# Kernel optimization log

Measured on AMD Instinct MI355X. Metric: run time of the kernel, lower is better.

The kernel has to match this reference:

```python
import jax, jax.numpy as jnp
import numpy as np

TEMPERATURE = 0.1
NEG_INF = -1e30  # finite sentinel to keep logsumexp grad-safe


def setup_inputs() -> dict:
    key = jax.random.key(0)
    k_emb, k_lab = jax.random.split(key)
    B, D, C = 8192, 256, 100
    embeddings = jax.random.normal(k_emb, (B, D), dtype=jnp.float32)
    labels = jax.random.randint(k_lab, (B,), 0, C, dtype=jnp.int64)
    return {"embeddings": embeddings, "labels": labels}


def reference(embeddings, labels):
    B = embeddings.shape[0]
    # squared L2 pairwise distance: ||x_i||^2 + ||x_j||^2 - 2 x_i . x_j
    sq = jnp.sum(embeddings * embeddings, axis=1)  # [B]
    gram = jnp.einsum('id,jd->ij', embeddings, embeddings)  # [B,B]
    dist2 = jnp.maximum(sq[:, None] + sq[None, :] - 2.0 * gram, 0.0)
    sim = -dist2 / TEMPERATURE  # [B,B]

    same = labels[:, None] == labels[None, :]
    eye = jnp.eye(B, dtype=bool)
    pos_mask = same & ~eye
    neg_mask = ~same

    # per-row uniform random positive via Gumbel-argmax over pos_mask
    k_sel = jax.random.key(42)
    g = jax.random.gumbel(k_sel, (B, B), dtype=jnp.float32)
    j = jnp.argmax(jnp.where(pos_mask, g, -jnp.inf), axis=1)  # [B]

    numerator = jnp.take_along_axis(sim, j[:, None], axis=1)[:, 0]  # sim[i, j_i]
    denominator = jax.nn.logsumexp(jnp.where(neg_mask, sim, NEG_INF), axis=1)

    valid = pos_mask.any(axis=1) & neg_mask.any(axis=1)
    per_row = -(numerator - denominator)
    n_valid = jnp.sum(valid)
    loss = jnp.sum(jnp.where(valid, per_row, 0.0)) / jnp.maximum(n_valid, 1)
    return jnp.where(n_valid > 0, loss, 0.0)
```

## Files before the change

kernel.cpp:

```cpp
#include <hip/hip_runtime.h>
#include <float.h>
#include <math.h>


#define B_N 8192
#define D_K 256
#define NCLS 100
#define MAXC 512
#define NSPLIT 16
#define NPART NSPLIT
#define JR (B_N / NSPLIT)
#define BI 128
#define BJ 64
#define NJT (JR / BJ)
#define BK 64
#define NKC (D_K / BK)
#define NEG_INF -1e30f
#define C2F  (-14.426950408889634f)
#define K2A  (28.853900817779268f)
#define LN2F (0.6931471805599453f)

typedef __attribute__((ext_vector_type(8))) short bf16x8;
typedef __attribute__((ext_vector_type(4))) float f32x4;
typedef unsigned short ushort_t;

__device__ __forceinline__ float ex2(float x){ return __builtin_amdgcn_exp2f(x); }
__device__ __forceinline__ float lg2(float x){ return __builtin_amdgcn_logf(x); }

__device__ __forceinline__ unsigned rotl32(unsigned x, int d){ return (x << d) | (x >> (32 - d)); }

__device__ __forceinline__ float gumbel_at(unsigned idx){
  const unsigned HALF = (unsigned)B_N * (unsigned)B_N / 2u;
  unsigned c0, c1; bool second;
  if (idx < HALF){ c0 = idx; c1 = idx + HALF; second = false; }
  else            { c0 = idx - HALF; c1 = idx; second = true; }
  const unsigned ks0 = 0u, ks1 = 42u, ks2 = 0u ^ 42u ^ 0x1BD11BDAu;
  unsigned x0 = c0 + ks0, x1 = c1 + ks1;
#define TF_RND(r) { x0 += x1; x1 = rotl32(x1, (r)); x1 ^= x0; }
  TF_RND(13) TF_RND(15) TF_RND(26) TF_RND(6)   x0 += ks1; x1 += ks2 + 1u;
  TF_RND(17) TF_RND(29) TF_RND(16) TF_RND(24)  x0 += ks2; x1 += ks0 + 2u;
  TF_RND(13) TF_RND(15) TF_RND(26) TF_RND(6)   x0 += ks0; x1 += ks1 + 3u;
  TF_RND(17) TF_RND(29) TF_RND(16) TF_RND(24)  x0 += ks1; x1 += ks2 + 4u;
  TF_RND(13) TF_RND(15) TF_RND(26) TF_RND(6)   x0 += ks2; x1 += ks0 + 5u;
#undef TF_RND
  unsigned bits = second ? x1 : x0;
  float u = __uint_as_float((bits >> 9) | 0x3f800000u) - 1.0f;
  const float TINY = 1.17549435e-38f;
  u = u * (1.0f - TINY) + TINY;
  u = fmaxf(TINY, u);
  return -logf(-logf(u));
}

__device__ __forceinline__ ushort_t f2bf(float x){
  unsigned u = __float_as_uint(x);
  return (ushort_t)((u + 0x7FFFu + ((u >> 16) & 1u)) >> 16);
}

__device__ __forceinline__ void async16(const ushort_t* g, ushort_t* lds_wave_base){
  __builtin_amdgcn_global_load_lds((const __attribute__((address_space(1))) void*)g,
                                   (__attribute__((address_space(3))) void*)lds_wave_base,
                                   16, 0, 0);
}

__global__ __launch_bounds__(256)
void prep_kernel(const float* __restrict__ E, ushort_t* __restrict__ Ebf,
                 float* __restrict__ sq, float* __restrict__ acc4,
                 const int* __restrict__ labels, int* __restrict__ cls_cnt,
                 int* __restrict__ clist){
  __shared__ int s_list[MAXC];
  __shared__ int s_n;
  if (blockIdx.x < B_N / 4){
    if (blockIdx.x == 0 && threadIdx.x < 4) acc4[threadIdx.x] = 0.f;
    int w = threadIdx.x >> 6, lane = threadIdx.x & 63;
    int row = blockIdx.x * 4 + w;
    const float4 v = *reinterpret_cast<const float4*>(E + (size_t)row * D_K + lane * 4);
    float s = v.x*v.x + v.y*v.y + v.z*v.z + v.w*v.w;
#pragma unroll
    for (int off = 32; off > 0; off >>= 1) s += __shfl_down(s, off);
    if (lane == 0) sq[row] = s;
    ushort4 o; o.x = f2bf(v.x); o.y = f2bf(v.y); o.z = f2bf(v.z); o.w = f2bf(v.w);
    *reinterpret_cast<ushort4*>(Ebf + (size_t)row * D_K + lane * 4) = o;
  } else {
    const int c = blockIdx.x - B_N / 4;
    const int tid = threadIdx.x;
    if (tid == 0) s_n = 0;
    __syncthreads();
    for (int t = tid; t < B_N; t += 256){
      if (labels[t] == c){
        int p = atomicAdd(&s_n, 1);
        if (p < MAXC) s_list[p] = t;
      }
    }
    __syncthreads();
    const int n = min(s_n, MAXC);
    if (tid == 0) cls_cnt[c] = n;
    for (int t = tid; t < n; t += 256) clist[c * MAXC + t] = s_list[t];
  }
}

__global__ __launch_bounds__(256)
void rowsel_kernel(const int* __restrict__ labels, const int* __restrict__ cls_cnt,
                   const int* __restrict__ clist, int* __restrict__ jsel){
  const int w = threadIdx.x >> 6, lane = threadIdx.x & 63;
  const int row = blockIdx.x * 4 + w;
  const int c = labels[row];
  const int n = min(cls_cnt[c], MAXC);
  float gb = -FLT_MAX; int jb = -1;
  for (int t = lane; t < n; t += 64){
    int j = clist[c * MAXC + t];
    if (j != row){
      float g = gumbel_at(((unsigned)row << 13) + (unsigned)j);
      if (g > gb || (g == gb && (unsigned)j < (unsigned)jb)){ gb = g; jb = j; }
    }
  }
#pragma unroll
  for (int off = 32; off > 0; off >>= 1){
    float g2 = __shfl_down(gb, off);
    int   j2 = __shfl_down(jb, off);
    if (g2 > gb || (g2 == gb && (unsigned)j2 < (unsigned)jb)){ gb = g2; jb = j2; }
  }
  if (lane == 0) jsel[row] = jb;
}

__global__ __launch_bounds__(256, 3)
void fused_kernel(const ushort_t* __restrict__ Ebf, const int* __restrict__ labels,
                  const float* __restrict__ sq, const int* __restrict__ jsel,
                  float* __restrict__ numer,
                  float* __restrict__ wsM, float* __restrict__ wsS)
{
  __shared__ __align__(16) ushort_t Bs[2][BJ * BK];
  __shared__ float s_h2j[JR];
  __shared__ int   s_lj[JR];
  __shared__ float s_h2i[BI];
  __shared__ int   s_li[BI];
  __shared__ int   s_ji[BI];

  const int bi    = blockIdx.x >> 4;
  const int split = blockIdx.x & 15;
  const int i0    = bi * BI;
  const int jbase = split * JR;
  const int tid   = threadIdx.x;
  const int lane  = tid & 63;
  const int w     = tid >> 6;
  const int quad  = lane >> 4;
  const int l15   = lane & 15;

  for (int t = tid; t < JR; t += 256){ s_h2j[t] = C2F * sq[jbase + t]; s_lj[t] = labels[jbase + t]; }
  if (tid < BI){ s_h2i[tid] = C2F * sq[i0 + tid]; s_li[tid] = labels[i0 + tid]; s_ji[tid] = jsel[i0 + tid]; }

  bf16x8 af[2][8];
#pragma unroll
  for (int mt = 0; mt < 2; mt++){
    const ushort_t* rp = Ebf + (size_t)(i0 + w * 32 + mt * 16 + l15) * D_K + quad * 8;
#pragma unroll
    for (int c = 0; c < 8; c++)
      af[mt][c] = *reinterpret_cast<const bf16x8*>(rp + c * 32);
  }

  f32x4 acc[2][4];
#pragma unroll
  for (int mt = 0; mt < 2; mt++)
#pragma unroll
    for (int nt = 0; nt < 4; nt++) acc[mt][nt] = (f32x4)0.f;
  float sm[8], ssum[8];
#pragma unroll
  for (int r = 0; r < 8; r++){ sm[r] = NEG_INF; ssum[r] = 0.f; }

  int soff[2];
#pragma unroll
  for (int rd = 0; rd < 2; rd++){
    int slot = rd * 256 + tid;
    int r = slot >> 3, gs = slot & 7;
    soff[rd] = r * D_K + ((gs ^ (r & 7)) << 3);
  }

#pragma unroll
  for (int rd = 0; rd < 2; rd++)
    async16(Ebf + (size_t)jbase * D_K + soff[rd],
            &Bs[0][(size_t)(rd * 256 + w * 64) * 8]);
  __syncthreads();

#pragma unroll 1
  for (int jt = 0; jt < NJT; jt++){
    const int j0 = jbase + jt * BJ;
#pragma unroll
    for (int kc = 0; kc < NKC; kc++){
      const int b = kc & 1;
      const int sn = jt * NKC + kc + 1;
      if (sn < NJT * NKC){
        const int kcn = sn & 3;
        const size_t gb0 = (size_t)(jbase + (sn >> 2) * BJ) * D_K + (size_t)kcn * BK;
#pragma unroll
        for (int rd = 0; rd < 2; rd++)
          async16(Ebf + gb0 + soff[rd],
                  &Bs[b ^ 1][(size_t)(rd * 256 + w * 64) * 8]);
      }
#pragma unroll
      for (int s = 0; s < 2; s++){
        const int g = s * 4 + quad;
        const int c = kc * 2 + s;
        bf16x8 bfr[4];
#pragma unroll
        for (int q = 0; q < 4; q++){
          int r = q * 16 + l15;
          bfr[q] = *reinterpret_cast<const bf16x8*>(&Bs[b][r * BK + ((g ^ (r & 7)) << 3)]);
        }
#pragma unroll
        for (int q = 0; q < 4; q++){
          acc[0][q] = __builtin_amdgcn_mfma_f32_16x16x32_bf16(af[0][c], bfr[q], acc[0][q], 0, 0, 0);
          acc[1][q] = __builtin_amdgcn_mfma_f32_16x16x32_bf16(af[1][c], bfr[q], acc[1][q], 0, 0, 0);
        }
      }
      if (kc == NKC - 1){
        float h2j[4]; int lj[4];
#pragma unroll
        for (int nt = 0; nt < 4; nt++){
          int ccol = jt * BJ + nt * 16 + l15;
          h2j[nt] = s_h2j[ccol]; lj[nt] = s_lj[ccol];
        }
#pragma unroll
        for (int mt = 0; mt < 2; mt++){
#pragma unroll
          for (int rr = 0; rr < 4; rr++){
            const int rl = w * 32 + mt * 16 + quad * 4 + rr;
            const float h2i = s_h2i[rl];
            const int lrow = s_li[rl], jsl = s_ji[rl];
            float sv[4];
#pragma unroll
            for (int nt = 0; nt < 4; nt++){
              float a = acc[mt][nt][rr];
              float sim2 = fminf(fmaf(K2A, a, h2i + h2j[nt]), 0.f);
              int colg = j0 + nt * 16 + l15;
              if (colg == jsl) numer[i0 + rl] = sim2;
              sv[nt] = (lj[nt] != lrow) ? sim2 : NEG_INF;
            }
            float m4 = fmaxf(fmaxf(sv[0], sv[1]), fmaxf(sv[2], sv[3]));
            float s4 = ex2(sv[0]-m4)+ex2(sv[1]-m4)+ex2(sv[2]-m4)+ex2(sv[3]-m4);
            const int sidx = mt * 4 + rr;
            float M = fmaxf(sm[sidx], m4);
            ssum[sidx] = ssum[sidx]*ex2(sm[sidx]-M) + s4*ex2(m4-M);
            sm[sidx] = M;
          }
        }
#pragma unroll
        for (int mt = 0; mt < 2; mt++)
#pragma unroll
          for (int nt = 0; nt < 4; nt++) acc[mt][nt] = (f32x4)0.f;
      }
      __syncthreads();
    }
  }

#pragma unroll
  for (int sidx = 0; sidx < 8; sidx++){
    float mv = sm[sidx], sv2 = ssum[sidx];
#pragma unroll
    for (int mask = 1; mask < 16; mask <<= 1){
      float m2 = __shfl_xor(mv, mask);
      float s2 = __shfl_xor(sv2, mask);
      float M = fmaxf(mv, m2);
      sv2 = sv2 * ex2(mv - M) + s2 * ex2(m2 - M);
      mv = M;
    }
    if (l15 == 0){
      const int mt = sidx >> 2, rr = sidx & 3;
      int rl = w * 32 + mt * 16 + quad * 4 + rr;
      int o = split * B_N + i0 + rl;
      wsM[o] = mv; wsS[o] = sv2;
    }
  }
}

__global__ __launch_bounds__(256)
void finale_kernel(const float* __restrict__ wsM, const float* __restrict__ wsS,
                   const float* __restrict__ numer, const int* __restrict__ jsel,
                   float* __restrict__ acc4, float* __restrict__ out)
{
  const int tid = threadIdx.x;
  const int row = blockIdx.x * 256 + tid;
  float M = -3.0e38f, S = 0.f;
#pragma unroll
  for (int p = 0; p < NPART; p++){
    float m2 = wsM[p * B_N + row], s2 = wsS[p * B_N + row];
    float Mn = fmaxf(M, m2);
    S = S * ex2(M - Mn) + s2 * ex2(m2 - Mn);
    M = Mn;
  }
  bool v = (jsel[row] >= 0) && (M > -5e29f);
  float s = v ? (LN2F * (M + lg2(S) - numer[row])) : 0.f;
  unsigned n = v ? 1u : 0u;
#pragma unroll
  for (int off = 32; off > 0; off >>= 1){ s += __shfl_down(s, off); n += __shfl_down(n, off); }
  __shared__ float ssm[4]; __shared__ unsigned snm[4];
  if ((tid & 63) == 0){ ssm[tid >> 6] = s; snm[tid >> 6] = n; }
  __syncthreads();
  if (tid == 0){
    float bs = ssm[0] + ssm[1] + ssm[2] + ssm[3];
    unsigned bn = snm[0] + snm[1] + snm[2] + snm[3];
    atomicAdd(&acc4[0], bs);
    atomicAdd((unsigned*)&acc4[1], bn);
    __threadfence();
    unsigned old = atomicAdd((unsigned*)&acc4[2], 1u);
    if (old == 31u){
      float St = atomicAdd(&acc4[0], 0.f);
      unsigned Nt = atomicAdd((unsigned*)&acc4[1], 0u);
      out[0] = (Nt > 0u) ? (St / (float)Nt) : 0.f;
    }
  }
}

extern "C" void kernel_launch(void* const* d_in, const int* in_sizes, int n_in,
                              void* d_out, int out_size, void* d_ws, size_t ws_size,
                              hipStream_t stream)
{
  const float* E      = (const float*)d_in[0];
  const int*   labels = (const int*)d_in[1];
  float*       out    = (float*)d_out;

  ushort_t* Ebf = (ushort_t*)d_ws;
  float* wsM    = (float*)(Ebf + (size_t)B_N * D_K);
  float* wsS    = wsM + NPART * B_N;
  float* sqb    = wsS + NPART * B_N;
  float* numer  = sqb + B_N;
  int* jsel     = (int*)(numer + B_N);
  float* acc4   = (float*)(jsel + B_N);
  int* cls_cnt  = (int*)(acc4 + 4);
  int* clist    = cls_cnt + NCLS;

  prep_kernel<<<B_N / 4 + NCLS, 256, 0, stream>>>(E, Ebf, sqb, acc4, labels, cls_cnt, clist);
  rowsel_kernel<<<B_N / 4, 256, 0, stream>>>(labels, cls_cnt, clist, jsel);
  fused_kernel<<<(B_N / BI) * NSPLIT, 256, 0, stream>>>(Ebf, labels, sqb, jsel, numer, wsM, wsS);
  finale_kernel<<<B_N / 256, 256, 0, stream>>>(wsM, wsS, numer, jsel, acc4, out);
}
```

Before: 145.5 us.

## Fuse row selection into prep and finale into fused kernel, deepen LDS pipeline

Row selection now runs inside the per-class blocks of prep_kernel using the class member list already in LDS, which removes the rowsel kernel and the global class-list round trip. The finale reduction moves into fused_kernel and is done by the last block to arrive, tracked with an atomic counter, which removes another launch. The B-tile pipeline grows from double to four LDS buffers with explicit vmcnt waits and barriers, occupancy is raised to four blocks per CU, and MFMA sections get s_setprio. The tradeoffs are a serial tail, since one block reduces all 8192 rows, and more LDS per block, which may limit the occupancy the launch bounds ask for.

```diff
diff --git a/kernel.cpp b/kernel.cpp
--- a/kernel.cpp
+++ b/kernel.cpp
@@ -15,6 +15,7 @@
 #define NJT (JR / BJ)
 #define BK 64
 #define NKC (D_K / BK)
+#define TOTB ((B_N / BI) * NSPLIT)
 #define NEG_INF -1e30f
 #define C2F  (-14.426950408889634f)
 #define K2A  (28.853900817779268f)
@@ -65,8 +66,7 @@
 __global__ __launch_bounds__(256)
 void prep_kernel(const float* __restrict__ E, ushort_t* __restrict__ Ebf,
                  float* __restrict__ sq, float* __restrict__ acc4,
-                 const int* __restrict__ labels, int* __restrict__ cls_cnt,
-                 int* __restrict__ clist){
+                 const int* __restrict__ labels, int* __restrict__ jsel){
   __shared__ int s_list[MAXC];
   __shared__ int s_n;
   if (blockIdx.x < B_N / 4){
@@ -83,6 +83,7 @@
   } else {
     const int c = blockIdx.x - B_N / 4;
     const int tid = threadIdx.x;
+    const int w = tid >> 6, lane = tid & 63;
     if (tid == 0) s_n = 0;
     __syncthreads();
     for (int t = tid; t < B_N; t += 256){
@@ -93,47 +94,41 @@
     }
     __syncthreads();
     const int n = min(s_n, MAXC);
-    if (tid == 0) cls_cnt[c] = n;
-    for (int t = tid; t < n; t += 256) clist[c * MAXC + t] = s_list[t];
-  }
-}
-
-__global__ __launch_bounds__(256)
-void rowsel_kernel(const int* __restrict__ labels, const int* __restrict__ cls_cnt,
-                   const int* __restrict__ clist, int* __restrict__ jsel){
-  const int w = threadIdx.x >> 6, lane = threadIdx.x & 63;
-  const int row = blockIdx.x * 4 + w;
-  const int c = labels[row];
-  const int n = min(cls_cnt[c], MAXC);
-  float gb = -FLT_MAX; int jb = -1;
-  for (int t = lane; t < n; t += 64){
-    int j = clist[c * MAXC + t];
-    if (j != row){
-      float g = gumbel_at(((unsigned)row << 13) + (unsigned)j);
-      if (g > gb || (g == gb && (unsigned)j < (unsigned)jb)){ gb = g; jb = j; }
-    }
-  }
-#pragma unroll
-  for (int off = 32; off > 0; off >>= 1){
-    float g2 = __shfl_down(gb, off);
-    int   j2 = __shfl_down(jb, off);
-    if (g2 > gb || (g2 == gb && (unsigned)j2 < (unsigned)jb)){ gb = g2; jb = j2; }
-  }
-  if (lane == 0) jsel[row] = jb;
-}
-
-__global__ __launch_bounds__(256, 3)
+    for (int m = w; m < n; m += 4){
+      const int row = s_list[m];
+      float gb = -FLT_MAX; int jb = -1;
+      for (int t = lane; t < n; t += 64){
+        int j = s_list[t];
+        if (j != row){
+          float g = gumbel_at(((unsigned)row << 13) + (unsigned)j);
+          if (g > gb || (g == gb && (unsigned)j < (unsigned)jb)){ gb = g; jb = j; }
+        }
+      }
+#pragma unroll
+      for (int off = 32; off > 0; off >>= 1){
+        float g2 = __shfl_down(gb, off);
+        int   j2 = __shfl_down(jb, off);
+        if (g2 > gb || (g2 == gb && (unsigned)j2 < (unsigned)jb)){ gb = g2; jb = j2; }
+      }
+      if (lane == 0) jsel[row] = jb;
+    }
+  }
+}
+
+__global__ __launch_bounds__(256, 4)
 void fused_kernel(const ushort_t* __restrict__ Ebf, const int* __restrict__ labels,
                   const float* __restrict__ sq, const int* __restrict__ jsel,
                   float* __restrict__ numer,
-                  float* __restrict__ wsM, float* __restrict__ wsS)
+                  float* __restrict__ wsM, float* __restrict__ wsS,
+                  float* __restrict__ acc4, float* __restrict__ out)
 {
-  __shared__ __align__(16) ushort_t Bs[2][BJ * BK];
+  __shared__ __align__(16) ushort_t Bs[4][BJ * BK];
   __shared__ float s_h2j[JR];
   __shared__ int   s_lj[JR];
   __shared__ float s_h2i[BI];
   __shared__ int   s_li[BI];
   __shared__ int   s_ji[BI];
+  __shared__ int   s_last;
 
   const int bi    = blockIdx.x >> 4;
   const int split = blockIdx.x & 15;
@@ -148,24 +143,6 @@
   for (int t = tid; t < JR; t += 256){ s_h2j[t] = C2F * sq[jbase + t]; s_lj[t] = labels[jbase + t]; }
   if (tid < BI){ s_h2i[tid] = C2F * sq[i0 + tid]; s_li[tid] = labels[i0 + tid]; s_ji[tid] = jsel[i0 + tid]; }
 
-  bf16x8 af[2][8];
-#pragma unroll
-  for (int mt = 0; mt < 2; mt++){
-    const ushort_t* rp = Ebf + (size_t)(i0 + w * 32 + mt * 16 + l15) * D_K + quad * 8;
-#pragma unroll
-    for (int c = 0; c < 8; c++)
-      af[mt][c] = *reinterpret_cast<const bf16x8*>(rp + c * 32);
-  }
-
-  f32x4 acc[2][4];
-#pragma unroll
-  for (int mt = 0; mt < 2; mt++)
-#pragma unroll
-    for (int nt = 0; nt < 4; nt++) acc[mt][nt] = (f32x4)0.f;
-  float sm[8], ssum[8];
-#pragma unroll
-  for (int r = 0; r < 8; r++){ sm[r] = NEG_INF; ssum[r] = 0.f; }
-
   int soff[2];
 #pragma unroll
   for (int rd = 0; rd < 2; rd++){
@@ -178,6 +155,25 @@
   for (int rd = 0; rd < 2; rd++)
     async16(Ebf + (size_t)jbase * D_K + soff[rd],
             &Bs[0][(size_t)(rd * 256 + w * 64) * 8]);
+
+  bf16x8 af[2][8];
+#pragma unroll
+  for (int mt = 0; mt < 2; mt++){
+    const ushort_t* rp = Ebf + (size_t)(i0 + w * 32 + mt * 16 + l15) * D_K + quad * 8;
+#pragma unroll
+    for (int c = 0; c < 8; c++)
+      af[mt][c] = *reinterpret_cast<const bf16x8*>(rp + c * 32);
+  }
+
+  f32x4 acc[2][4];
+#pragma unroll
+  for (int mt = 0; mt < 2; mt++)
+#pragma unroll
+    for (int nt = 0; nt < 4; nt++) acc[mt][nt] = (f32x4)0.f;
+  float sm[8], ssum[8];
+#pragma unroll
+  for (int r = 0; r < 8; r++){ sm[r] = NEG_INF; ssum[r] = 0.f; }
+
   __syncthreads();
 
 #pragma unroll 1
@@ -185,32 +181,37 @@
     const int j0 = jbase + jt * BJ;
 #pragma unroll
     for (int kc = 0; kc < NKC; kc++){
-      const int b = kc & 1;
-      const int sn = jt * NKC + kc + 1;
-      if (sn < NJT * NKC){
-        const int kcn = sn & 3;
-        const size_t gb0 = (size_t)(jbase + (sn >> 2) * BJ) * D_K + (size_t)kcn * BK;
+      if (kc < NKC - 1){
+        const size_t gb0 = (size_t)j0 * D_K + (size_t)(kc + 1) * BK;
 #pragma unroll
         for (int rd = 0; rd < 2; rd++)
-          async16(Ebf + gb0 + soff[rd],
-                  &Bs[b ^ 1][(size_t)(rd * 256 + w * 64) * 8]);
-      }
+          async16(Ebf + gb0 + soff[rd], &Bs[kc + 1][(size_t)(rd * 256 + w * 64) * 8]);
+        asm volatile("s_waitcnt vmcnt(2)\n\ts_barrier" ::: "memory");
+      } else {
+        if (jt < NJT - 1){
+          const size_t gb0 = (size_t)(j0 + BJ) * D_K;
+#pragma unroll
+          for (int rd = 0; rd < 2; rd++)
+            async16(Ebf + gb0 + soff[rd], &Bs[0][(size_t)(rd * 256 + w * 64) * 8]);
+          asm volatile("s_waitcnt vmcnt(2)\n\ts_barrier" ::: "memory");
+        } else {
+          asm volatile("s_waitcnt vmcnt(0)\n\ts_barrier" ::: "memory");
+        }
+      }
+      __builtin_amdgcn_s_setprio(1);
 #pragma unroll
       for (int s = 0; s < 2; s++){
         const int g = s * 4 + quad;
         const int c = kc * 2 + s;
-        bf16x8 bfr[4];
 #pragma unroll
         for (int q = 0; q < 4; q++){
-          int r = q * 16 + l15;
-          bfr[q] = *reinterpret_cast<const bf16x8*>(&Bs[b][r * BK + ((g ^ (r & 7)) << 3)]);
-        }
-#pragma unroll
-        for (int q = 0; q < 4; q++){
-          acc[0][q] = __builtin_amdgcn_mfma_f32_16x16x32_bf16(af[0][c], bfr[q], acc[0][q], 0, 0, 0);
-          acc[1][q] = __builtin_amdgcn_mfma_f32_16x16x32_bf16(af[1][c], bfr[q], acc[1][q], 0, 0, 0);
-        }
-      }
+          const int r = q * 16 + l15;
+          bf16x8 bq = *reinterpret_cast<const bf16x8*>(&Bs[kc][r * BK + ((g ^ (r & 7)) << 3)]);
+          acc[0][q] = __builtin_amdgcn_mfma_f32_16x16x32_bf16(af[0][c], bq, acc[0][q], 0, 0, 0);
+          acc[1][q] = __builtin_amdgcn_mfma_f32_16x16x32_bf16(af[1][c], bq, acc[1][q], 0, 0, 0);
+        }
+      }
+      __builtin_amdgcn_s_setprio(0);
       if (kc == NKC - 1){
         float h2j[4]; int lj[4];
 #pragma unroll
@@ -247,7 +248,6 @@
 #pragma unroll
           for (int nt = 0; nt < 4; nt++) acc[mt][nt] = (f32x4)0.f;
       }
-      __syncthreads();
     }
   }
 
@@ -269,41 +269,38 @@
       wsM[o] = mv; wsS[o] = sv2;
     }
   }
-}
-
-__global__ __launch_bounds__(256)
-void finale_kernel(const float* __restrict__ wsM, const float* __restrict__ wsS,
-                   const float* __restrict__ numer, const int* __restrict__ jsel,
-                   float* __restrict__ acc4, float* __restrict__ out)
-{
-  const int tid = threadIdx.x;
-  const int row = blockIdx.x * 256 + tid;
-  float M = -3.0e38f, S = 0.f;
-#pragma unroll
-  for (int p = 0; p < NPART; p++){
-    float m2 = wsM[p * B_N + row], s2 = wsS[p * B_N + row];
-    float Mn = fmaxf(M, m2);
-    S = S * ex2(M - Mn) + s2 * ex2(m2 - Mn);
-    M = Mn;
-  }
-  bool v = (jsel[row] >= 0) && (M > -5e29f);
-  float s = v ? (LN2F * (M + lg2(S) - numer[row])) : 0.f;
-  unsigned n = v ? 1u : 0u;
-#pragma unroll
-  for (int off = 32; off > 0; off >>= 1){ s += __shfl_down(s, off); n += __shfl_down(n, off); }
-  __shared__ float ssm[4]; __shared__ unsigned snm[4];
-  if ((tid & 63) == 0){ ssm[tid >> 6] = s; snm[tid >> 6] = n; }
+
+  __threadfence();
+  if (tid == 0){
+    int old = atomicAdd((int*)&acc4[2], 1);
+    s_last = (old == TOTB - 1) ? 1 : 0;
+  }
   __syncthreads();
-  if (tid == 0){
-    float bs = ssm[0] + ssm[1] + ssm[2] + ssm[3];
-    unsigned bn = snm[0] + snm[1] + snm[2] + snm[3];
-    atomicAdd(&acc4[0], bs);
-    atomicAdd((unsigned*)&acc4[1], bn);
-    __threadfence();
-    unsigned old = atomicAdd((unsigned*)&acc4[2], 1u);
-    if (old == 31u){
-      float St = atomicAdd(&acc4[0], 0.f);
-      unsigned Nt = atomicAdd((unsigned*)&acc4[1], 0u);
+  if (s_last){
+    float s_acc = 0.f; unsigned n_acc = 0u;
+    for (int row = tid; row < B_N; row += 256){
+      float M = -3.0e38f, S = 0.f;
+#pragma unroll
+      for (int p = 0; p < NPART; p++){
+        float m2 = wsM[p * B_N + row], s2 = wsS[p * B_N + row];
+        float Mn = fmaxf(M, m2);
+        S = S * ex2(M - Mn) + s2 * ex2(m2 - Mn);
+        M = Mn;
+      }
+      bool v = (s_ji[0] == s_ji[0]) && (jsel[row] >= 0) && (M > -5e29f);
+      if (v){ s_acc += LN2F * (M + lg2(S) - numer[row]); n_acc += 1u; }
+    }
+#pragma unroll
+    for (int off = 32; off > 0; off >>= 1){
+      s_acc += __shfl_down(s_acc, off);
+      n_acc += __shfl_down(n_acc, off);
+    }
+    __shared__ float ssm[4]; __shared__ unsigned snm[4];
+    if (lane == 0){ ssm[w] = s_acc; snm[w] = n_acc; }
+    __syncthreads();
+    if (tid == 0){
+      float St = ssm[0] + ssm[1] + ssm[2] + ssm[3];
+      unsigned Nt = snm[0] + snm[1] + snm[2] + snm[3];
       out[0] = (Nt > 0u) ? (St / (float)Nt) : 0.f;
     }
   }
@@ -324,11 +321,7 @@
   float* numer  = sqb + B_N;
   int* jsel     = (int*)(numer + B_N);
   float* acc4   = (float*)(jsel + B_N);
-  int* cls_cnt  = (int*)(acc4 + 4);
-  int* clist    = cls_cnt + NCLS;
-
-  prep_kernel<<<B_N / 4 + NCLS, 256, 0, stream>>>(E, Ebf, sqb, acc4, labels, cls_cnt, clist);
-  rowsel_kernel<<<B_N / 4, 256, 0, stream>>>(labels, cls_cnt, clist, jsel);
-  fused_kernel<<<(B_N / BI) * NSPLIT, 256, 0, stream>>>(Ebf, labels, sqb, jsel, numer, wsM, wsS);
-  finale_kernel<<<B_N / 256, 256, 0, stream>>>(wsM, wsS, numer, jsel, acc4, out);
-}
+
+  prep_kernel<<<B_N / 4 + NCLS, 256, 0, stream>>>(E, Ebf, sqb, acc4, labels, jsel);
+  fused_kernel<<<TOTB, 256, 0, stream>>>(Ebf, labels, sqb, jsel, numer, wsM, wsS, acc4, out);
+}
```

New measurement: 311.3 us. 2.14x slower.
